# Performance work log

Measured on AMD Instinct MI355X. Metric: run time of the kernel, lower is better.

## Reference

```python
import jax, jax.numpy as jnp
import numpy as np

REGION_NUM = 8  # DRConv2d default region_num


def setup_inputs() -> dict:
    key = jax.random.key(0)
    ks = jax.random.split(key, 10)
    B, H, W = 4, 256, 256
    C = 64   # n_fea_middle
    r = REGION_NUM
    s = 0.05
    return {
        "rgb":  jax.random.normal(ks[0], (B, 3, H, W), jnp.float32),
        "edge": jax.random.normal(ks[1], (B, 1, H, W), jnp.float32),
        # conv1: 1x1, 4 -> C
        "W1":  jax.random.normal(ks[2], (C, 4), jnp.float32) * s,
        "b1":  jax.random.normal(ks[3], (C,), jnp.float32) * s,
        # DRConv kernel-generator stage 1: Conv2d(C, r*r, 1)
        "Wk1": jax.random.normal(ks[4], (r * r, C), jnp.float32) * s,
        "bk1": jax.random.normal(ks[5], (r * r,), jnp.float32) * s,
        # stage 2: Conv2d(r*r, r*C*C, 1, groups=r) -> per group: r inputs, C*C outputs
        "Wk2": jax.random.normal(ks[6], (r, C * C, r), jnp.float32) * s,
        "bk2": jax.random.normal(ks[7], (r, C * C), jnp.float32) * s,
        # conv_guide: Conv2d(C, r, 1)
        "Wg":  jax.random.normal(ks[8], (r, C), jnp.float32) * s,
        "bg":  jax.random.normal(ks[9], (r,), jnp.float32) * s,
    }


def reference(rgb, edge, W1, b1, Wk1, bk1, Wk2, bk2, Wg, bg):
    r = REGION_NUM
    B = rgb.shape[0]
    # concat rgb+edge, 1x1 conv to n_fea_middle
    x = jnp.concatenate([rgb, edge], axis=1)                       # B,4,H,W
    x1 = jnp.einsum('bihw,oi->bohw', x, W1) + b1[None, :, None, None]  # B,C,H,W
    C = x1.shape[1]
    # ---- DRConv2d(C, C, kernel_size=1, region_num=r) ----
    # kernel-generating branch: AdaptiveAvgPool2d(1) == global mean for k=1
    g = jnp.mean(x1, axis=(2, 3))                                  # B,C
    t = jax.nn.sigmoid(g @ Wk1.T + bk1)                            # B,r*r
    tg = t.reshape(B, r, r)                                        # grouped 1x1 conv, groups=r
    k = jnp.einsum('bgi,goi->bgo', tg, Wk2) + bk2[None]            # B,r,C*C
    kernel = k.reshape(B, r, C, C)                                 # B,r,Cout,Cin
    # cross-correlation: per-batch, per-region 1x1 conv of x1 with generated kernel
    region_out = jnp.einsum('bchw,broc->brohw', x1, kernel)        # B,r,Cout,H,W
    # guide branch + hard region routing (asign_index forward)
    guide = jnp.einsum('bchw,rc->brhw', x1, Wg) + bg[None, :, None, None]  # B,r,H,W
    mask = jax.nn.one_hot(jnp.argmax(guide, axis=1), r, axis=1, dtype=x1.dtype)  # B,r,H,W
    out = jnp.sum(region_out * mask[:, :, None], axis=1)           # B,Cout,H,W
    return out
```

## Files before the change

kernel.cpp:

```cpp
#include <hip/hip_runtime.h>
#include <hip/hip_bf16.h>


#define HW_ 65536

__device__ double g_part[128];
__device__ double g_tD[256];
__device__ double g_WgP[32];
__device__ double g_bgP[8];
__device__ float  g_Wm[8192];
__device__ float  g_Bm[2048];

__global__ void k_sum(const float* __restrict__ rgb, const float* __restrict__ edge) {
    int plane = blockIdx.x;
    int chunk = blockIdx.y;
    int b = plane >> 2, ch = plane & 3;
    const float* src = (ch < 3) ? rgb + (size_t)(b * 3 + ch) * HW_
                                : edge + (size_t)b * HW_;
    src += chunk * 8192;
    int t = threadIdx.x;
    double s = 0.0;
    #pragma unroll
    for (int p = 0; p < 8; ++p) {
        float4 v = *(const float4*)(src + (p * 256 + t) * 4);
        s += (double)v.x + (double)v.y + (double)v.z + (double)v.w;
    }
    #pragma unroll
    for (int off = 32; off; off >>= 1) s += __shfl_down(s, off);
    __shared__ double wsum[4];
    if ((t & 63) == 0) wsum[t >> 6] = s;
    __syncthreads();
    if (t == 0) g_part[plane * 8 + chunk] = wsum[0] + wsum[1] + wsum[2] + wsum[3];
}

__global__ void k_params_a(const float* __restrict__ W1, const float* __restrict__ b1,
                           const float* __restrict__ Wk1, const float* __restrict__ bk1,
                           const float* __restrict__ Wg, const float* __restrict__ bg) {
    __shared__ double xm[16];
    __shared__ double g[256];
    int t = threadIdx.x;
    if (t < 16) {
        double s = 0;
        #pragma unroll
        for (int i = 0; i < 8; ++i) s += g_part[t * 8 + i];
        xm[t] = s * (1.0 / 65536.0);
    }
    __syncthreads();
    {
        int b = t >> 6, c = t & 63;
        double acc = (double)b1[c];
        #pragma unroll
        for (int j = 0; j < 4; ++j)
            acc += (double)W1[c * 4 + j] * xm[b * 4 + j];
        g[t] = acc;
    }
    __syncthreads();
    {
        int b = t >> 6, j = t & 63;
        double z = (double)bk1[j];
        for (int c = 0; c < 64; ++c)
            z += (double)Wk1[j * 64 + c] * g[b * 64 + c];
        g_tD[t] = 1.0 / (1.0 + exp(-z));
    }
    if (t < 32) {
        int r = t >> 2, j = t & 3;
        double a = 0;
        for (int c = 0; c < 64; ++c)
            a += (double)Wg[r * 64 + c] * (double)W1[c * 4 + j];
        g_WgP[t] = a;
    } else if (t < 40) {
        int r = t - 32;
        double a = (double)bg[r];
        for (int c = 0; c < 64; ++c)
            a += (double)Wg[r * 64 + c] * (double)b1[c];
        g_bgP[r] = a;
    }
}

__global__ void k_params_b(const float* __restrict__ W1, const float* __restrict__ b1,
                           const float* __restrict__ Wk2, const float* __restrict__ bk2) {
    int blk = blockIdx.x;
    int b = blk >> 3, gr = blk & 7;
    int o = threadIdx.x;
    double tt[8];
    #pragma unroll
    for (int i = 0; i < 8; ++i) tt[i] = g_tD[b * 64 + gr * 8 + i];
    double aw0 = 0, aw1 = 0, aw2 = 0, aw3 = 0, ab = 0;
    const float* wk2p = Wk2 + ((size_t)gr * 4096 + o * 64) * 8;
    const float* bk2p = bk2 + (size_t)gr * 4096 + o * 64;
    for (int c = 0; c < 64; ++c) {
        double ker = (double)bk2p[c];
        #pragma unroll
        for (int i = 0; i < 8; ++i)
            ker += tt[i] * (double)wk2p[c * 8 + i];
        aw0 += ker * (double)W1[c * 4 + 0];
        aw1 += ker * (double)W1[c * 4 + 1];
        aw2 += ker * (double)W1[c * 4 + 2];
        ab  += ker * (double)b1[c];
        aw3 += ker * (double)W1[c * 4 + 3];
    }
    float* w = g_Wm + ((size_t)blk * 64 + o) * 4;
    w[0] = (float)aw0; w[1] = (float)aw1; w[2] = (float)aw2; w[3] = (float)aw3;
    g_Bm[blk * 64 + o] = (float)ab;
}

__launch_bounds__(256)
__global__ void k_main(const float* __restrict__ rgb, const float* __restrict__ edge,
                       float* __restrict__ out) {
    __shared__ __align__(16) float sW[8 * 1028];
    __shared__ __align__(16) float sB[8 * 68];
    __shared__ double sWg[32];
    __shared__ double sBg[8];
    int t = threadIdx.x;
    int b = blockIdx.y;

    {
        const float4* src = (const float4*)(g_Wm + (size_t)b * 2048);
        #pragma unroll
        for (int k = 0; k < 2; ++k) {
            int idx = t + 256 * k; int r = idx >> 6, o = idx & 63;
            *(float4*)&sW[r * 1028 + o * 4] = src[idx];
        }
        const float* bs = g_Bm + (size_t)b * 512;
        #pragma unroll
        for (int k = 0; k < 2; ++k) {
            int idx = t + 256 * k; int r = idx >> 6, o = idx & 63;
            sB[r * 68 + o] = bs[idx];
        }
        if (t < 32) sWg[t] = g_WgP[t];
        else if (t < 40) sBg[t - 32] = g_bgP[t - 32];
    }
    __syncthreads();

    float wg[32], bgf[8];
    #pragma unroll
    for (int i = 0; i < 32; ++i) wg[i] = (float)sWg[i];
    #pragma unroll
    for (int r = 0; r < 8; ++r) bgf[r] = (float)sBg[r];

    int pxb = (blockIdx.x * 256 + t) * 4;
    float xa[4], xb[4], xc[4], xd[4];
    {
        float4 v0 = *(const float4*)(rgb  + (size_t)(b * 3 + 0) * HW_ + pxb);
        float4 v1 = *(const float4*)(rgb  + (size_t)(b * 3 + 1) * HW_ + pxb);
        float4 v2 = *(const float4*)(rgb  + (size_t)(b * 3 + 2) * HW_ + pxb);
        float4 v3 = *(const float4*)(edge + (size_t)b * HW_ + pxb);
        xa[0] = v0.x; xa[1] = v0.y; xa[2] = v0.z; xa[3] = v0.w;
        xb[0] = v1.x; xb[1] = v1.y; xb[2] = v1.z; xb[3] = v1.w;
        xc[0] = v2.x; xc[1] = v2.y; xc[2] = v2.z; xc[3] = v2.w;
        xd[0] = v3.x; xd[1] = v3.y; xd[2] = v3.z; xd[3] = v3.w;
    }

    int reg[4];
    #pragma unroll
    for (int p = 0; p < 4; ++p) {
        float m1 = -1e30f, m2 = -1e30f; int bi = 0;
        #pragma unroll
        for (int r = 0; r < 8; ++r) {
            float gv = bgf[r] + wg[r * 4 + 0] * xa[p] + wg[r * 4 + 1] * xb[p]
                              + wg[r * 4 + 2] * xc[p] + wg[r * 4 + 3] * xd[p];
            if (gv > m1) { m2 = m1; m1 = gv; bi = r; }
            else if (gv > m2) { m2 = gv; }
        }
        if (m1 - m2 < 1e-4f) {
            double da = xa[p], db = xb[p], dc = xc[p], dd = xd[p];
            double bm = -1e300; bi = 0;
            #pragma unroll
            for (int r = 0; r < 8; ++r) {
                double gv = sBg[r] + sWg[r * 4 + 0] * da + sWg[r * 4 + 1] * db
                                   + sWg[r * 4 + 2] * dc + sWg[r * 4 + 3] * dd;
                if (gv > bm) { bm = gv; bi = r; }
            }
        }
        reg[p] = bi;
    }

    int base[4], bbase[4];
    #pragma unroll
    for (int p = 0; p < 4; ++p) { base[p] = reg[p] * 1028; bbase[p] = reg[p] * 68; }

    float* outp = out + (size_t)b * 64 * HW_ + pxb;
    #pragma unroll 4
    for (int oq = 0; oq < 16; ++oq) {
        float res[4][4];
        #pragma unroll
        for (int p = 0; p < 4; ++p) {
            float4 bq = *(const float4*)&sB[bbase[p] + oq * 4];
            float bqa[4] = {bq.x, bq.y, bq.z, bq.w};
            #pragma unroll
            for (int k = 0; k < 4; ++k) {
                float4 w = *(const float4*)&sW[base[p] + (oq * 4 + k) * 4];
                res[k][p] = bqa[k] + w.x * xa[p] + w.y * xb[p]
                                   + w.z * xc[p] + w.w * xd[p];
            }
        }
        #pragma unroll
        for (int k = 0; k < 4; ++k) {
            int o = oq * 4 + k;
            float4 pk; pk.x = res[k][0]; pk.y = res[k][1];
            pk.z = res[k][2]; pk.w = res[k][3];
            *(float4*)(outp + (size_t)o * HW_) = pk;
        }
    }
}

extern "C" void kernel_launch(void* const* d_in, const int* in_sizes, int n_in,
                              void* d_out, int out_size, void* d_ws, size_t ws_size,
                              hipStream_t stream) {
    (void)d_ws; (void)ws_size;
    const float* rgb  = (const float*)d_in[0];
    const float* edge = (const float*)d_in[1];
    const float* W1   = (const float*)d_in[2];
    const float* b1   = (const float*)d_in[3];
    const float* Wk1  = (const float*)d_in[4];
    const float* bk1  = (const float*)d_in[5];
    const float* Wk2  = (const float*)d_in[6];
    const float* bk2  = (const float*)d_in[7];
    const float* Wg   = (const float*)d_in[8];
    const float* bg   = (const float*)d_in[9];
    float* out = (float*)d_out;

    k_sum<<<dim3(16, 8), 256, 0, stream>>>(rgb, edge);
    k_params_a<<<1, 256, 0, stream>>>(W1, b1, Wk1, bk1, Wg, bg);
    k_params_b<<<32, 64, 0, stream>>>(W1, b1, Wk2, bk2);
    k_main<<<dim3(64, 4), 256, 0, stream>>>(rgb, edge, out);
}
```

Before: 133.8 us.

## Fuse param kernels, split main kernel over output-channel quarters, nontemporal stores

Merges the two parameter kernels into one 32-block kernel. Each block now recomputes its own sigmoid gate slice and splits the 64-channel reduction across 4 thread groups, combining them through shared memory. The main kernel gains a z-dimension of 4, so each block writes 16 output channels, giving 4x more blocks and a smaller shared footprint. Output stores become nontemporal. The cost is that each pixel's region argmax and input loads are now repeated 4 times, once per channel group.

After: 113.0 us. 1.18x faster.

```diff
diff --git a/kernel.cpp b/kernel.cpp
--- a/kernel.cpp
+++ b/kernel.cpp
@@ -1,15 +1,15 @@
 #include <hip/hip_runtime.h>
-#include <hip/hip_bf16.h>
 
 
 #define HW_ 65536
 
 __device__ double g_part[128];
-__device__ double g_tD[256];
 __device__ double g_WgP[32];
 __device__ double g_bgP[8];
-__device__ float  g_Wm[8192];
-__device__ float  g_Bm[2048];
+__device__ __align__(16) float g_Wm[8192];
+__device__ __align__(16) float g_Bm[2048];
+
+typedef float f4v __attribute__((ext_vector_type(4)));
 
 __global__ void k_sum(const float* __restrict__ rgb, const float* __restrict__ edge) {
     int plane = blockIdx.x;
@@ -33,12 +33,18 @@
     if (t == 0) g_part[plane * 8 + chunk] = wsum[0] + wsum[1] + wsum[2] + wsum[3];
 }
 
-__global__ void k_params_a(const float* __restrict__ W1, const float* __restrict__ b1,
-                           const float* __restrict__ Wk1, const float* __restrict__ bk1,
-                           const float* __restrict__ Wg, const float* __restrict__ bg) {
+__global__ void k_params(const float* __restrict__ W1, const float* __restrict__ b1,
+                         const float* __restrict__ Wk1, const float* __restrict__ bk1,
+                         const float* __restrict__ Wk2, const float* __restrict__ bk2,
+                         const float* __restrict__ Wg, const float* __restrict__ bg) {
+    int blk = blockIdx.x;
+    int b = blk >> 3, gr = blk & 7;
+    int t = threadIdx.x;
     __shared__ double xm[16];
-    __shared__ double g[256];
-    int t = threadIdx.x;
+    __shared__ double gsh[64];
+    __shared__ double tt_sh[8];
+    __shared__ double red[4][64][5];
+
     if (t < 16) {
         double s = 0;
         #pragma unroll
@@ -46,49 +52,44 @@
         xm[t] = s * (1.0 / 65536.0);
     }
     __syncthreads();
-    {
-        int b = t >> 6, c = t & 63;
-        double acc = (double)b1[c];
-        #pragma unroll
-        for (int j = 0; j < 4; ++j)
-            acc += (double)W1[c * 4 + j] * xm[b * 4 + j];
-        g[t] = acc;
-    }
-    __syncthreads();
-    {
-        int b = t >> 6, j = t & 63;
+    if (t < 64) {
+        double acc = (double)b1[t];
+        #pragma unroll
+        for (int j = 0; j < 4; ++j) acc += (double)W1[t * 4 + j] * xm[b * 4 + j];
+        gsh[t] = acc;
+    }
+    __syncthreads();
+    if (t < 8) {
+        int j = gr * 8 + t;
         double z = (double)bk1[j];
-        for (int c = 0; c < 64; ++c)
-            z += (double)Wk1[j * 64 + c] * g[b * 64 + c];
-        g_tD[t] = 1.0 / (1.0 + exp(-z));
-    }
-    if (t < 32) {
-        int r = t >> 2, j = t & 3;
-        double a = 0;
-        for (int c = 0; c < 64; ++c)
-            a += (double)Wg[r * 64 + c] * (double)W1[c * 4 + j];
-        g_WgP[t] = a;
-    } else if (t < 40) {
-        int r = t - 32;
-        double a = (double)bg[r];
-        for (int c = 0; c < 64; ++c)
-            a += (double)Wg[r * 64 + c] * (double)b1[c];
-        g_bgP[r] = a;
-    }
-}
-
-__global__ void k_params_b(const float* __restrict__ W1, const float* __restrict__ b1,
-                           const float* __restrict__ Wk2, const float* __restrict__ bk2) {
-    int blk = blockIdx.x;
-    int b = blk >> 3, gr = blk & 7;
-    int o = threadIdx.x;
+        for (int c = 0; c < 64; ++c) z += (double)Wk1[j * 64 + c] * gsh[c];
+        tt_sh[t] = 1.0 / (1.0 + exp(-z));
+    }
+    if (blk == 0) {
+        if (t >= 64 && t < 96) {
+            int r = (t - 64) >> 2, j = (t - 64) & 3;
+            double a = 0;
+            for (int c = 0; c < 64; ++c)
+                a += (double)Wg[r * 64 + c] * (double)W1[c * 4 + j];
+            g_WgP[t - 64] = a;
+        } else if (t >= 96 && t < 104) {
+            int r = t - 96;
+            double a = (double)bg[r];
+            for (int c = 0; c < 64; ++c)
+                a += (double)Wg[r * 64 + c] * (double)b1[c];
+            g_bgP[r] = a;
+        }
+    }
+    __syncthreads();
+
+    int o = t & 63, cq = t >> 6;
     double tt[8];
     #pragma unroll
-    for (int i = 0; i < 8; ++i) tt[i] = g_tD[b * 64 + gr * 8 + i];
+    for (int i = 0; i < 8; ++i) tt[i] = tt_sh[i];
     double aw0 = 0, aw1 = 0, aw2 = 0, aw3 = 0, ab = 0;
     const float* wk2p = Wk2 + ((size_t)gr * 4096 + o * 64) * 8;
     const float* bk2p = bk2 + (size_t)gr * 4096 + o * 64;
-    for (int c = 0; c < 64; ++c) {
+    for (int c = cq * 16; c < cq * 16 + 16; ++c) {
         double ker = (double)bk2p[c];
         #pragma unroll
         for (int i = 0; i < 8; ++i)
@@ -99,33 +100,42 @@
         ab  += ker * (double)b1[c];
         aw3 += ker * (double)W1[c * 4 + 3];
     }
-    float* w = g_Wm + ((size_t)blk * 64 + o) * 4;
-    w[0] = (float)aw0; w[1] = (float)aw1; w[2] = (float)aw2; w[3] = (float)aw3;
-    g_Bm[blk * 64 + o] = (float)ab;
+    red[cq][o][0] = aw0; red[cq][o][1] = aw1; red[cq][o][2] = aw2;
+    red[cq][o][3] = aw3; red[cq][o][4] = ab;
+    __syncthreads();
+    if (t < 64) {
+        double w0 = 0, w1 = 0, w2 = 0, w3 = 0, bb = 0;
+        #pragma unroll
+        for (int q = 0; q < 4; ++q) {
+            w0 += red[q][t][0]; w1 += red[q][t][1]; w2 += red[q][t][2];
+            w3 += red[q][t][3]; bb += red[q][t][4];
+        }
+        float* w = g_Wm + ((size_t)blk * 64 + t) * 4;
+        w[0] = (float)w0; w[1] = (float)w1; w[2] = (float)w2; w[3] = (float)w3;
+        g_Bm[blk * 64 + t] = (float)bb;
+    }
 }
 
 __launch_bounds__(256)
 __global__ void k_main(const float* __restrict__ rgb, const float* __restrict__ edge,
                        float* __restrict__ out) {
-    __shared__ __align__(16) float sW[8 * 1028];
-    __shared__ __align__(16) float sB[8 * 68];
+    __shared__ __align__(16) float sW[8 * 68];
+    __shared__ __align__(16) float sB[8 * 20];
     __shared__ double sWg[32];
     __shared__ double sBg[8];
     int t = threadIdx.x;
     int b = blockIdx.y;
+    int z = blockIdx.z;
 
     {
-        const float4* src = (const float4*)(g_Wm + (size_t)b * 2048);
-        #pragma unroll
-        for (int k = 0; k < 2; ++k) {
-            int idx = t + 256 * k; int r = idx >> 6, o = idx & 63;
-            *(float4*)&sW[r * 1028 + o * 4] = src[idx];
-        }
-        const float* bs = g_Bm + (size_t)b * 512;
-        #pragma unroll
-        for (int k = 0; k < 2; ++k) {
-            int idx = t + 256 * k; int r = idx >> 6, o = idx & 63;
-            sB[r * 68 + o] = bs[idx];
+        if (t < 128) {
+            int r = t >> 4, ol = t & 15;
+            const float4* src = (const float4*)g_Wm;
+            *(float4*)&sW[r * 68 + ol * 4] = src[(size_t)(b * 8 + r) * 64 + z * 16 + ol];
+        } else {
+            int idx = t - 128;
+            int r = idx >> 4, ol = idx & 15;
+            sB[r * 20 + ol] = g_Bm[(size_t)(b * 8 + r) * 64 + z * 16 + ol];
         }
         if (t < 32) sWg[t] = g_WgP[t];
         else if (t < 40) sBg[t - 32] = g_bgP[t - 32];
@@ -177,11 +187,11 @@
 
     int base[4], bbase[4];
     #pragma unroll
-    for (int p = 0; p < 4; ++p) { base[p] = reg[p] * 1028; bbase[p] = reg[p] * 68; }
-
-    float* outp = out + (size_t)b * 64 * HW_ + pxb;
-    #pragma unroll 4
-    for (int oq = 0; oq < 16; ++oq) {
+    for (int p = 0; p < 4; ++p) { base[p] = reg[p] * 68; bbase[p] = reg[p] * 20; }
+
+    float* outp = out + (size_t)(b * 64 + z * 16) * HW_ + pxb;
+    #pragma unroll
+    for (int oq = 0; oq < 4; ++oq) {
         float res[4][4];
         #pragma unroll
         for (int p = 0; p < 4; ++p) {
@@ -196,10 +206,9 @@
         }
         #pragma unroll
         for (int k = 0; k < 4; ++k) {
-            int o = oq * 4 + k;
-            float4 pk; pk.x = res[k][0]; pk.y = res[k][1];
+            f4v pk; pk.x = res[k][0]; pk.y = res[k][1];
             pk.z = res[k][2]; pk.w = res[k][3];
-            *(float4*)(outp + (size_t)o * HW_) = pk;
+            __builtin_nontemporal_store(pk, (f4v*)(outp + (size_t)(oq * 4 + k) * HW_));
         }
     }
 }
@@ -221,7 +230,6 @@
     float* out = (float*)d_out;
 
     k_sum<<<dim3(16, 8), 256, 0, stream>>>(rgb, edge);
-    k_params_a<<<1, 256, 0, stream>>>(W1, b1, Wk1, bk1, Wg, bg);
-    k_params_b<<<32, 64, 0, stream>>>(W1, b1, Wk2, bk2);
-    k_main<<<dim3(64, 4), 256, 0, stream>>>(rgb, edge, out);
-}
+    k_params<<<32, 256, 0, stream>>>(W1, b1, Wk1, bk1, Wk2, bk2, Wg, bg);
+    k_main<<<dim3(64, 4, 4), 256, 0, stream>>>(rgb, edge, out);
+}
```
